# Performance work log

Measured on AMD Instinct MI355X. Metric: run time of the kernel, lower is better.

## Reference

```python
import jax, jax.numpy as jnp
import numpy as np

N, E, ET = 20000, 200000, 40000
D_IN, H, NEA, HL, OUT = 8, 128, 7, 128, 4
HC = H * NEA  # 896


def _init(k, shape, fan_in):
    return jax.random.normal(k, shape, jnp.float32) * (1.0 / np.sqrt(fan_in))


def setup_inputs() -> dict:
    key = jax.random.key(0)
    ks = list(jax.random.split(key, 16))
    return {
        "x": jax.random.normal(ks[0], (N, D_IN), jnp.float32),
        "edge_index": jax.random.randint(ks[1], (2, E), 0, N),
        "edge_attr": jax.random.uniform(ks[2], (E, NEA), jnp.float32),
        "edge_index_test": jax.random.randint(ks[3], (2, ET), 0, N),
        "W0": _init(ks[4], (NEA, D_IN, H), D_IN), "b0": jnp.zeros((NEA, H), jnp.float32),
        "W1": _init(ks[5], (HC, H), HC), "b1": jnp.zeros((H,), jnp.float32),
        "W2": _init(ks[6], (NEA, H, H), H), "b2": jnp.zeros((NEA, H), jnp.float32),
        "W3": _init(ks[7], (NEA, HC, H), HC), "b3": jnp.zeros((NEA, H), jnp.float32),
        "ew1": _init(ks[8], (NEA, NEA * 4), NEA), "eb1": jnp.zeros((NEA * 4,), jnp.float32),
        "ew2": _init(ks[9], (NEA * 4, NEA * 4), NEA * 4), "eb2": jnp.zeros((NEA * 4,), jnp.float32),
        "ew3": _init(ks[10], (NEA * 4, 1), NEA * 4), "eb3": jnp.zeros((1,), jnp.float32),
        "lw0": _init(ks[11], (2 * HC, HL), 2 * HC), "lb0": jnp.zeros((HL,), jnp.float32),
        "lwh": _init(ks[12], (3, HL, HL), HL), "lbh": jnp.zeros((3, HL), jnp.float32),
        "lw4": _init(ks[13], (HL, OUT), HL), "lb4": jnp.zeros((OUT,), jnp.float32),
    }


def _forward(x, edge_attr, W0, b0, W1, b1, W2, b2, W3, b3,
             ew1, eb1, ew2, eb2, ew3, eb3,
             lw0, lb0, lwh, lbh, lw4, lb4,
             edge_index, edge_index_test):
    n = x.shape[0]
    row, col = edge_index[0], edge_index[1]
    loop = jnp.arange(n)
    # PyG gcn_norm: append self-loops with weight 1
    rows = jnp.concatenate([row, loop])
    cols = jnp.concatenate([col, loop])

    def gcn_norm(w):
        w2 = jnp.concatenate([w, jnp.ones((n,), w.dtype)])
        deg = jax.ops.segment_sum(w2, cols, num_segments=n)
        dis = jnp.where(deg > 0, 1.0 / jnp.sqrt(deg), 0.0)
        return dis[rows] * w2 * dis[cols]  # [E+N]

    norms = [gcn_norm(edge_attr[:, i]) for i in range(NEA)]

    def conv(h, W, b, norm):
        m = (h @ W)[rows] * norm[:, None]  # [E+N, H] gathered messages
        return jax.ops.segment_sum(m, cols, num_segments=n) + b

    x1 = jax.nn.relu(jnp.concatenate([conv(x, W0[i], b0[i], norms[i]) for i in range(NEA)], -1))
    # multi_edge_to_one (edge_fc_layers[1]) -> scalar edge weight in (0,1)
    t = jax.nn.relu(edge_attr @ ew1 + eb1)
    t = jax.nn.relu(t @ ew2 + eb2)
    ew = jax.nn.sigmoid((t @ ew3 + eb3)[:, 0])
    x2 = jax.nn.relu(conv(x1, W1, b1, gcn_norm(ew)))
    x3 = jax.nn.relu(jnp.concatenate([conv(x2, W2[i], b2[i], norms[i]) for i in range(NEA)], -1))
    x4 = jax.nn.relu(jnp.concatenate([conv(x3, W3[i], b3[i], norms[i]) for i in range(NEA)], -1))
    # dropout(p=0.5) is identity in eval mode

    def link_mlp(e):
        h = jax.nn.relu(e @ lw0 + lb0)
        for i in range(3):
            h = jax.nn.relu(h @ lwh[i] + lbh[i])
        return h @ lw4 + lb4

    s, d = edge_index_test[0], edge_index_test[1]
    t1 = link_mlp(jnp.concatenate([x4[s], x4[d]], -1))
    t2 = link_mlp(jnp.concatenate([x4[d], x4[s]], -1))[:, jnp.array([0, 2, 1, 3])]
    return 0.5 * (t1 + t2)  # [E_test, 4]


def reference(x, edge_index, edge_attr, edge_index_test,
              W0, b0, W1, b1, W2, b2, W3, b3,
              ew1, eb1, ew2, eb2, ew3, eb3,
              lw0, lb0, lwh, lbh, lw4, lb4):
    return _forward(x, edge_attr, W0, b0, W1, b1, W2, b2, W3, b3,
                    ew1, eb1, ew2, eb2, ew3, eb3,
                    lw0, lb0, lwh, lbh, lw4, lb4,
                    edge_index, edge_index_test)
```

## Files before the change

kernel.cpp:

```cpp
#include <hip/hip_runtime.h>
#include <math.h>

#define NN 20000
#define NE 200000
#define NT 40000

typedef _Float16 f16;
typedef __attribute__((ext_vector_type(8))) _Float16 f16x8;
typedef __attribute__((ext_vector_type(4))) float f32x4;
typedef __attribute__((ext_vector_type(2))) _Float16 h2;

__device__ __forceinline__ void split_store_h(float v, f16* hi, f16* lo, size_t idx) {
  f16 h = (f16)v;
  hi[idx] = h;
  lo[idx] = (f16)(v - (float)h);
}

__global__ void k_edge_mlp(const float* __restrict__ ea,
                           const float* __restrict__ w1, const float* __restrict__ b1,
                           const float* __restrict__ w2, const float* __restrict__ b2,
                           const float* __restrict__ w3, const float* __restrict__ b3,
                           float* __restrict__ out) {
  int e = blockIdx.x * 256 + threadIdx.x;
  if (e >= NE) return;
  float a[7];
#pragma unroll
  for (int i = 0; i < 7; i++) a[i] = ea[e * 7 + i];
  float t1[28];
#pragma unroll
  for (int j = 0; j < 28; j++) {
    float s = b1[j];
#pragma unroll
    for (int k = 0; k < 7; k++) s = fmaf(a[k], w1[k * 28 + j], s);
    t1[j] = fmaxf(s, 0.f);
  }
  float t2[28];
  for (int j = 0; j < 28; j++) {
    float s = b2[j];
    for (int k = 0; k < 28; k++) s = fmaf(t1[k], w2[k * 28 + j], s);
    t2[j] = fmaxf(s, 0.f);
  }
  float s = b3[0];
  for (int k = 0; k < 28; k++) s = fmaf(t2[k], w3[k], s);
  out[e] = 1.f / (1.f + expf(-s));
}

__global__ void k_count(const int* __restrict__ col, int* __restrict__ cnt) {
  int e = blockIdx.x * 256 + threadIdx.x;
  if (e < NE) atomicAdd(&cnt[col[e]], 1);
}

__global__ void k_scan(const int* __restrict__ cnt, int* __restrict__ rowptr) {
  __shared__ int sums[256];
  __shared__ int offs[256];
  int t = threadIdx.x;
  const int CH = (NN + 255) / 256;
  int base = t * CH;
  int s = 0;
  for (int i = 0; i < CH; i++) { int idx = base + i; if (idx < NN) s += cnt[idx]; }
  sums[t] = s;
  __syncthreads();
  if (t == 0) {
    int acc = 0;
    for (int i = 0; i < 256; i++) { offs[i] = acc; acc += sums[i]; }
    rowptr[NN] = acc;
  }
  __syncthreads();
  int acc = offs[t];
  for (int i = 0; i < CH; i++) {
    int idx = base + i;
    if (idx < NN) { rowptr[idx] = acc; acc += cnt[idx]; }
  }
}

__global__ void k_copy_i32(const int* __restrict__ src, int* __restrict__ dst, int n) {
  int i = blockIdx.x * 256 + threadIdx.x;
  if (i < n) dst[i] = src[i];
}

__global__ void k_fill_csr(const int* __restrict__ col, int* __restrict__ cursor,
                           int* __restrict__ eid) {
  int e = blockIdx.x * 256 + threadIdx.x;
  if (e >= NE) return;
  int pos = atomicAdd(&cursor[col[e]], 1);
  eid[pos] = e;
}

__global__ __launch_bounds__(64) void k_deg_csr(const int* __restrict__ rowptr,
                                                const int* __restrict__ eid,
                                                const float* __restrict__ ea,
                                                const float* __restrict__ ewb,
                                                float* __restrict__ dis) {
  int t = threadIdx.x;
  int n = blockIdx.x * 8 + (t >> 3);
  int i = t & 7;
  if (n >= NN) return;
  float deg = 1.f;
  int s = rowptr[n], e2 = rowptr[n + 1];
  for (int p = s; p < e2; p++) {
    int e = eid[p];
    deg += (i < 7) ? ea[e * 7 + i] : ewb[e];
  }
  dis[i * NN + n] = rsqrtf(deg);
}

__global__ void k_csr_norms(const int* __restrict__ eid, const int* __restrict__ row,
                            const int* __restrict__ col, const float* __restrict__ ea,
                            const float* __restrict__ ew, const float* __restrict__ dis,
                            int* __restrict__ csr_src, float* __restrict__ csr_norm) {
  int p = blockIdx.x * 256 + threadIdx.x;
  if (p >= NE) return;
  int e = eid[p];
  int r = row[e], c = col[e];
  csr_src[p] = r;
#pragma unroll
  for (int i = 0; i < 7; i++)
    csr_norm[i * NE + p] = dis[i * NN + r] * ea[e * 7 + i] * dis[i * NN + c];
  csr_norm[7 * NE + p] = dis[7 * NN + r] * ew[e] * dis[7 * NN + c];
}

__global__ void k_wprep(const float* __restrict__ W, int ldW, size_t matOff, int K,
                        f16* __restrict__ WT) {
  int g = blockIdx.y;
  int idx = blockIdx.x * 256 + threadIdx.x;
  if (idx >= K * 128) return;
  int k = idx >> 7, n = idx & 127;
  float v = W[(size_t)g * matOff + (size_t)k * ldW + n];
  WT[(size_t)g * 128 * K + (size_t)n * K + k] = (f16)v;
}

template <int OUTM, bool RELU, bool BIAS, bool GROUP_A, bool SWIZZLE>
__global__ __launch_bounds__(256) void k_mgemm(
    const f16* __restrict__ Ahi, const f16* __restrict__ Alo,
    const f16* __restrict__ BT,
    const float* __restrict__ bias,
    float* __restrict__ Cf, f16* __restrict__ Chi, f16* __restrict__ Clo,
    f16* __restrict__ Ch,
    int ldA, int M, int K, int NG, int GXp) {
  int rowT, g;
  if (SWIZZLE) {
    int b = blockIdx.x;
    int xcd = b & 7, s = b >> 3;
    g = s % NG;
    int lr = s / NG;
    rowT = lr * 8 + xcd;
    if (rowT >= GXp) return;
  } else {
    rowT = blockIdx.x;
    g = blockIdx.y;
  }
  __shared__ f16 smem[12288];
  const int tid = threadIdx.x;
  const int w = tid >> 6, lane = tid & 63;
  const int quad = lane >> 4, lc = lane & 15;
  const int wr = w >> 1, wc = w & 1;
  const int bm = rowT * 128;
  const int ldC = NG * 128;
  const int cb = g * 128;
  const int aoff = GROUP_A ? g * K : 0;
  const f16* Bg = BT + (size_t)g * 128 * K;
  const int srow = lane >> 2, skoff = (lane & 3) * 8;

  f32x4 acc[4][4] = {};

  for (int k0 = 0; k0 < K; k0 += 32) {
#pragma unroll
    for (int l = 0; l < 6; l++) {
      int c = w + l * 4;
      int t = c >> 3, r16 = c & 7;
      int rowi = r16 * 16 + srow;
      f16* ldst = smem + t * 4096 + r16 * 512;
      const f16* src;
      if (t < 2) {
        int gm = bm + rowi;
        if (gm > M - 1) gm = M - 1;
        src = (t == 0 ? Ahi : Alo) + (size_t)gm * ldA + aoff + k0 + skoff;
      } else {
        src = Bg + (size_t)rowi * K + k0 + skoff;
      }
      __builtin_amdgcn_global_load_lds(
          (const __attribute__((address_space(1))) void*)src,
          (__attribute__((address_space(3))) void*)ldst, 16, 0, 0);
    }
    __syncthreads();
    f16x8 bf[4];
#pragma unroll
    for (int nt = 0; nt < 4; nt++) {
      int r = wc * 64 + nt * 16 + lc;
      bf[nt] = *(const f16x8*)(smem + 2 * 4096 + r * 32 + quad * 8);
    }
#pragma unroll
    for (int mt = 0; mt < 4; mt++) {
      int r = wr * 64 + mt * 16 + lc;
      f16x8 ah = *(const f16x8*)(smem + 0 * 4096 + r * 32 + quad * 8);
      f16x8 al = *(const f16x8*)(smem + 1 * 4096 + r * 32 + quad * 8);
#pragma unroll
      for (int nt = 0; nt < 4; nt++) {
        acc[mt][nt] = __builtin_amdgcn_mfma_f32_16x16x32_f16(ah, bf[nt], acc[mt][nt], 0, 0, 0);
        acc[mt][nt] = __builtin_amdgcn_mfma_f32_16x16x32_f16(al, bf[nt], acc[mt][nt], 0, 0, 0);
      }
    }
    __syncthreads();
  }

  float bv[4];
  if (BIAS) {
#pragma unroll
    for (int nt = 0; nt < 4; nt++) bv[nt] = bias[cb + wc * 64 + nt * 16 + lc];
  }
#pragma unroll
  for (int mt = 0; mt < 4; mt++) {
#pragma unroll
    for (int r = 0; r < 4; r++) {
      int gm = bm + wr * 64 + mt * 16 + quad * 4 + r;
      if (gm >= M) continue;
#pragma unroll
      for (int nt = 0; nt < 4; nt++) {
        float v = acc[mt][nt][r];
        if (BIAS) v += bv[nt];
        if (RELU) v = fmaxf(v, 0.f);
        size_t idx = (size_t)gm * ldC + cb + wc * 64 + nt * 16 + lc;
        if (OUTM == 1) {
          f16 h = (f16)v;
          Chi[idx] = h;
          Clo[idx] = (f16)(v - (float)h);
        } else if (OUTM == 2) {
          Ch[idx] = (f16)v;
        } else {
          Cf[idx] = v;
        }
      }
    }
  }
}

__global__ __launch_bounds__(448) void k_agg7(const f16* __restrict__ hW,
                                              const float* __restrict__ csr_norm,
                                              const float* __restrict__ dis,
                                              const int* __restrict__ rowptr,
                                              const int* __restrict__ csr_src,
                                              const float* __restrict__ bias,
                                              f16* __restrict__ outhi,
                                              f16* __restrict__ outlo) {
  int n = blockIdx.x;
  int f2 = threadIdx.x;
  int i = f2 >> 6;
  const h2* hw2 = (const h2*)hW;
  const float* nrm = csr_norm + (size_t)i * NE;
  float d = dis[i * NN + n];
  h2 sv = hw2[(size_t)n * 448 + f2];
  float ax = d * d * (float)sv.x, ay = d * d * (float)sv.y;
  int s = rowptr[n], e = rowptr[n + 1];
  int p = s;
  for (; p + 4 <= e; p += 4) {
    int s0 = csr_src[p], s1 = csr_src[p + 1], s2 = csr_src[p + 2], s3 = csr_src[p + 3];
    float n0 = nrm[p], n1 = nrm[p + 1], n2 = nrm[p + 2], n3 = nrm[p + 3];
    h2 v0 = hw2[(size_t)s0 * 448 + f2];
    h2 v1 = hw2[(size_t)s1 * 448 + f2];
    h2 v2 = hw2[(size_t)s2 * 448 + f2];
    h2 v3 = hw2[(size_t)s3 * 448 + f2];
    ax = fmaf(n0, (float)v0.x, ax); ay = fmaf(n0, (float)v0.y, ay);
    ax = fmaf(n1, (float)v1.x, ax); ay = fmaf(n1, (float)v1.y, ay);
    ax = fmaf(n2, (float)v2.x, ax); ay = fmaf(n2, (float)v2.y, ay);
    ax = fmaf(n3, (float)v3.x, ax); ay = fmaf(n3, (float)v3.y, ay);
  }
  for (; p < e; p++) {
    int s0 = csr_src[p];
    float n0 = nrm[p];
    h2 v0 = hw2[(size_t)s0 * 448 + f2];
    ax = fmaf(n0, (float)v0.x, ax); ay = fmaf(n0, (float)v0.y, ay);
  }
  float vx = fmaxf(ax + bias[2 * f2], 0.f);
  float vy = fmaxf(ay + bias[2 * f2 + 1], 0.f);
  split_store_h(vx, outhi, outlo, (size_t)n * 896 + 2 * f2);
  split_store_h(vy, outhi, outlo, (size_t)n * 896 + 2 * f2 + 1);
}

__global__ __launch_bounds__(256) void k_agg1(const f16* __restrict__ hW,
                                              const float* __restrict__ nrm,
                                              const float* __restrict__ dis_i,
                                              const int* __restrict__ rowptr,
                                              const int* __restrict__ csr_src,
                                              const float* __restrict__ bias,
                                              float* __restrict__ x2f) {
  int t = threadIdx.x;
  int n = blockIdx.x * 4 + (t >> 6);
  int f2 = t & 63;
  if (n >= NN) return;
  const h2* hw2 = (const h2*)hW;
  float d = dis_i[n];
  h2 sv = hw2[(size_t)n * 64 + f2];
  float ax = d * d * (float)sv.x, ay = d * d * (float)sv.y;
  int s = rowptr[n], e = rowptr[n + 1];
  int p = s;
  for (; p + 4 <= e; p += 4) {
    int s0 = csr_src[p], s1 = csr_src[p + 1], s2 = csr_src[p + 2], s3 = csr_src[p + 3];
    float n0 = nrm[p], n1 = nrm[p + 1], n2 = nrm[p + 2], n3 = nrm[p + 3];
    h2 v0 = hw2[(size_t)s0 * 64 + f2];
    h2 v1 = hw2[(size_t)s1 * 64 + f2];
    h2 v2 = hw2[(size_t)s2 * 64 + f2];
    h2 v3 = hw2[(size_t)s3 * 64 + f2];
    ax = fmaf(n0, (float)v0.x, ax); ay = fmaf(n0, (float)v0.y, ay);
    ax = fmaf(n1, (float)v1.x, ax); ay = fmaf(n1, (float)v1.y, ay);
    ax = fmaf(n2, (float)v2.x, ax); ay = fmaf(n2, (float)v2.y, ay);
    ax = fmaf(n3, (float)v3.x, ax); ay = fmaf(n3, (float)v3.y, ay);
  }
  for (; p < e; p++) {
    int s0 = csr_src[p];
    float n0 = nrm[p];
    h2 v0 = hw2[(size_t)s0 * 64 + f2];
    ax = fmaf(n0, (float)v0.x, ax); ay = fmaf(n0, (float)v0.y, ay);
  }
  x2f[(size_t)n * 128 + 2 * f2] = fmaxf(ax + bias[2 * f2], 0.f);
  x2f[(size_t)n * 128 + 2 * f2 + 1] = fmaxf(ay + bias[2 * f2 + 1], 0.f);
}

__global__ __launch_bounds__(256) void k_agg2(const float* __restrict__ x2f,
                                              const float* __restrict__ csr_norm,
                                              const float* __restrict__ dis,
                                              const int* __restrict__ rowptr,
                                              const int* __restrict__ csr_src,
                                              f16* __restrict__ ohi,
                                              f16* __restrict__ olo) {
  int t = threadIdx.x;
  int n = blockIdx.x * 4 + (t >> 6);
  int f2 = t & 63;
  if (n >= NN) return;
  const float2* x2 = (const float2*)x2f;
  float2 sv = x2[(size_t)n * 64 + f2];
  float ax[7], ay[7];
#pragma unroll
  for (int i = 0; i < 7; i++) {
    float d = dis[i * NN + n];
    ax[i] = d * d * sv.x;
    ay[i] = d * d * sv.y;
  }
  int s = rowptr[n], e = rowptr[n + 1];
  int p = s;
  for (; p + 2 <= e; p += 2) {
    int s0 = csr_src[p], s1 = csr_src[p + 1];
    float2 v0 = x2[(size_t)s0 * 64 + f2];
    float2 v1 = x2[(size_t)s1 * 64 + f2];
#pragma unroll
    for (int i = 0; i < 7; i++) {
      float n0 = csr_norm[(size_t)i * NE + p];
      float n1 = csr_norm[(size_t)i * NE + p + 1];
      ax[i] = fmaf(n0, v0.x, ax[i]); ay[i] = fmaf(n0, v0.y, ay[i]);
      ax[i] = fmaf(n1, v1.x, ax[i]); ay[i] = fmaf(n1, v1.y, ay[i]);
    }
  }
  for (; p < e; p++) {
    int s0 = csr_src[p];
    float2 v0 = x2[(size_t)s0 * 64 + f2];
#pragma unroll
    for (int i = 0; i < 7; i++) {
      float n0 = csr_norm[(size_t)i * NE + p];
      ax[i] = fmaf(n0, v0.x, ax[i]); ay[i] = fmaf(n0, v0.y, ay[i]);
    }
  }
#pragma unroll
  for (int i = 0; i < 7; i++) {
    split_store_h(ax[i], ohi, olo, (size_t)n * 896 + i * 128 + 2 * f2);
    split_store_h(ay[i], ohi, olo, (size_t)n * 896 + i * 128 + 2 * f2 + 1);
  }
}

__global__ __launch_bounds__(64) void k_agg_x(const float* __restrict__ x,
                                              const float* __restrict__ csr_norm,
                                              const float* __restrict__ dis,
                                              const int* __restrict__ rowptr,
                                              const int* __restrict__ csr_src,
                                              float* __restrict__ xagg) {
  int n = blockIdx.x;
  int f = threadIdx.x;
  if (f >= 56) return;
  int i = f >> 3, c = f & 7;
  float d = dis[i * NN + n];
  float acc = d * d * x[(size_t)n * 8 + c];
  int s = rowptr[n], e = rowptr[n + 1];
  for (int p = s; p < e; p++)
    acc = fmaf(csr_norm[i * NE + p], x[(size_t)csr_src[p] * 8 + c], acc);
  xagg[(size_t)n * 56 + f] = acc;
}

__global__ __launch_bounds__(896) void k_gemm0(const float* __restrict__ xagg,
                                               const float* __restrict__ W0,
                                               const float* __restrict__ b0,
                                               f16* __restrict__ outhi,
                                               f16* __restrict__ outlo) {
  int n = blockIdx.x;
  int f = threadIdx.x;
  int i = f >> 7, h = f & 127;
  float s = b0[i * 128 + h];
#pragma unroll
  for (int c = 0; c < 8; c++)
    s = fmaf(xagg[(size_t)n * 56 + i * 8 + c], W0[(i * 8 + c) * 128 + h], s);
  float v = fmaxf(s, 0.f);
  split_store_h(v, outhi, outlo, (size_t)n * 896 + f);
}

__global__ __launch_bounds__(128) void k_link_gather(const float* __restrict__ UV,
                                                     const int* __restrict__ eit,
                                                     const float* __restrict__ lb0,
                                                     f16* __restrict__ Hhi,
                                                     f16* __restrict__ Hlo) {
  int t = blockIdx.x;
  int f = threadIdx.x;
  int s = eit[t], d = eit[NT + t];
  float b = lb0[f];
  float v1 = fmaxf(UV[(size_t)s * 256 + f] + UV[(size_t)d * 256 + 128 + f] + b, 0.f);
  float v2 = fmaxf(UV[(size_t)d * 256 + f] + UV[(size_t)s * 256 + 128 + f] + b, 0.f);
  split_store_h(v1, Hhi, Hlo, (size_t)t * 128 + f);
  split_store_h(v2, Hhi, Hlo, (size_t)(NT + t) * 128 + f);
}

__global__ void k_link_out(const f16* __restrict__ Hhi, const f16* __restrict__ Hlo,
                           const float* __restrict__ lw4, const float* __restrict__ lb4,
                           float* __restrict__ out) {
  int t = blockIdx.x * 256 + threadIdx.x;
  if (t >= NT) return;
  float o1[4] = {lb4[0], lb4[1], lb4[2], lb4[3]};
  float o2[4] = {o1[0], o1[1], o1[2], o1[3]};
  for (int k = 0; k < 128; k++) {
    size_t i1 = (size_t)t * 128 + k, i2 = (size_t)(NT + t) * 128 + k;
    float h1 = (float)Hhi[i1] + (float)Hlo[i1];
    float h2v = (float)Hhi[i2] + (float)Hlo[i2];
#pragma unroll
    for (int j = 0; j < 4; j++) {
      float w = lw4[k * 4 + j];
      o1[j] = fmaf(h1, w, o1[j]);
      o2[j] = fmaf(h2v, w, o2[j]);
    }
  }
  out[t * 4 + 0] = 0.5f * (o1[0] + o2[0]);
  out[t * 4 + 1] = 0.5f * (o1[1] + o2[2]);
  out[t * 4 + 2] = 0.5f * (o1[2] + o2[1]);
  out[t * 4 + 3] = 0.5f * (o1[3] + o2[3]);
}

extern "C" void kernel_launch(void* const* d_in, const int* in_sizes, int n_in,
                              void* d_out, int out_size, void* d_ws, size_t ws_size,
                              hipStream_t stream) {
  const float* x   = (const float*)d_in[0];
  const int*   ei  = (const int*)d_in[1];
  const float* ea  = (const float*)d_in[2];
  const int*   eit = (const int*)d_in[3];
  const float* W0  = (const float*)d_in[4];
  const float* b0  = (const float*)d_in[5];
  const float* W1  = (const float*)d_in[6];
  const float* b1  = (const float*)d_in[7];
  const float* W2  = (const float*)d_in[8];
  const float* b2  = (const float*)d_in[9];
  const float* W3  = (const float*)d_in[10];
  const float* b3  = (const float*)d_in[11];
  const float* ew1 = (const float*)d_in[12];
  const float* eb1 = (const float*)d_in[13];
  const float* ew2 = (const float*)d_in[14];
  const float* eb2 = (const float*)d_in[15];
  const float* ew3 = (const float*)d_in[16];
  const float* eb3 = (const float*)d_in[17];
  const float* lw0 = (const float*)d_in[18];
  const float* lb0 = (const float*)d_in[19];
  const float* lwh = (const float*)d_in[20];
  const float* lbh = (const float*)d_in[21];
  const float* lw4 = (const float*)d_in[22];
  const float* lb4 = (const float*)d_in[23];
  const int* row = ei;
  const int* col = ei + NE;
  float* out = (float*)d_out;

  char* ws = (char*)d_ws;
  size_t off = 0;
  auto alloc = [&](size_t bytes) -> char* {
    char* p = ws + off;
    off += (bytes + 255) & ~(size_t)255;
    return p;
  };
  f16*   xAhi   = (f16*)alloc((size_t)NN * 896 * 2);
  f16*   xAlo   = (f16*)alloc((size_t)NN * 896 * 2);
  float* xB     = (float*)alloc((size_t)NN * 896 * 4);
  float* x2f    = (float*)alloc((size_t)NN * 128 * 4);
  float* UV     = (float*)alloc((size_t)NN * 256 * 4);
  float* csr_nrm= (float*)alloc((size_t)8 * NE * 4);
  float* dis    = (float*)alloc((size_t)8 * NN * 4);
  float* ewb    = (float*)alloc((size_t)NE * 4);
  int*   rowptr = (int*)alloc((size_t)(NN + 1) * 4);
  int*   cursor = (int*)alloc((size_t)NN * 4);
  int*   eid    = (int*)alloc((size_t)NE * 4);
  int*   csr_src= (int*)alloc((size_t)NE * 4);
  f16* w1t  = (f16*)alloc((size_t)128 * 896 * 2);
  f16* w2t  = (f16*)alloc((size_t)7 * 128 * 128 * 2);
  f16* w3t  = (f16*)alloc((size_t)7 * 128 * 896 * 2);
  f16* lw0t = (f16*)alloc((size_t)2 * 128 * 896 * 2);
  f16* lwht = (f16*)alloc((size_t)3 * 128 * 128 * 2);
  float* xagg = UV;
  (void)ws_size; (void)in_sizes; (void)n_in; (void)out_size;

  const int EB = (NE + 255) / 256;
  const int NB = (NN + 255) / 256;
  const int GX = (NN + 127) / 128;
  const int MC = (GX + 7) / 8;

  k_wprep<<<dim3(448, 1), 256, 0, stream>>>(W1, 128, 0, 896, w1t);
  k_wprep<<<dim3(64, 7), 256, 0, stream>>>(W2, 128, (size_t)128 * 128, 128, w2t);
  k_wprep<<<dim3(448, 7), 256, 0, stream>>>(W3, 128, (size_t)896 * 128, 896, w3t);
  k_wprep<<<dim3(448, 2), 256, 0, stream>>>(lw0, 128, (size_t)896 * 128, 896, lw0t);
  k_wprep<<<dim3(64, 3), 256, 0, stream>>>(lwh, 128, (size_t)128 * 128, 128, lwht);

  k_edge_mlp<<<EB, 256, 0, stream>>>(ea, ew1, eb1, ew2, eb2, ew3, eb3, ewb);
  hipMemsetAsync(cursor, 0, (size_t)NN * 4, stream);
  k_count<<<EB, 256, 0, stream>>>(col, cursor);
  k_scan<<<1, 256, 0, stream>>>(cursor, rowptr);
  k_copy_i32<<<NB, 256, 0, stream>>>(rowptr, cursor, NN);
  k_fill_csr<<<EB, 256, 0, stream>>>(col, cursor, eid);
  k_deg_csr<<<(NN + 7) / 8, 64, 0, stream>>>(rowptr, eid, ea, ewb, dis);
  k_csr_norms<<<EB, 256, 0, stream>>>(eid, row, col, ea, ewb, dis, csr_src, csr_nrm);

  k_agg_x<<<NN, 64, 0, stream>>>(x, csr_nrm, dis, rowptr, csr_src, xagg);
  k_gemm0<<<NN, 896, 0, stream>>>(xagg, W0, b0, xAhi, xAlo);

  f16* hW1 = (f16*)xB;
  k_mgemm<2, false, false, false, false><<<dim3(GX, 1), 256, 0, stream>>>(
      xAhi, xAlo, w1t, nullptr, nullptr, nullptr, nullptr, hW1,
      896, NN, 896, 1, GX);
  k_agg1<<<(NN + 3) / 4, 256, 0, stream>>>(hW1, csr_nrm + (size_t)7 * NE,
                                           dis + (size_t)7 * NN, rowptr, csr_src, b1, x2f);

  f16* xagg2hi = (f16*)xB;
  f16* xagg2lo = xagg2hi + (size_t)NN * 896;
  k_agg2<<<(NN + 3) / 4, 256, 0, stream>>>(x2f, csr_nrm, dis, rowptr, csr_src,
                                           xagg2hi, xagg2lo);
  k_mgemm<1, true, true, true, false><<<dim3(GX, 7), 256, 0, stream>>>(
      xagg2hi, xagg2lo, w2t, b2, nullptr, xAhi, xAlo, nullptr,
      896, NN, 128, 7, GX);

  f16* hW3 = (f16*)xB;
  k_mgemm<2, false, false, false, true><<<dim3(8 * MC * 7), 256, 0, stream>>>(
      xAhi, xAlo, w3t, nullptr, nullptr, nullptr, nullptr, hW3,
      896, NN, 896, 7, GX);
  k_agg7<<<NN, 448, 0, stream>>>(hW3, csr_nrm, dis, rowptr, csr_src, b3, xAhi, xAlo);

  k_mgemm<0, false, false, false, true><<<dim3(8 * MC * 2), 256, 0, stream>>>(
      xAhi, xAlo, lw0t, nullptr, UV, nullptr, nullptr, nullptr,
      896, NN, 896, 2, GX);

  f16* Hahi = (f16*)xB;
  f16* Halo = Hahi + (size_t)2 * NT * 128;
  f16* Hbhi = Halo + (size_t)2 * NT * 128;
  f16* Hblo = Hbhi + (size_t)2 * NT * 128;
  k_link_gather<<<NT, 128, 0, stream>>>(UV, eit, lb0, Hahi, Halo);
  const int LGX = (2 * NT + 127) / 128;
  for (int i = 0; i < 3; i++) {
    const f16* wt = lwht + (size_t)i * 128 * 128;
    const float* bb = lbh + (size_t)i * 128;
    f16* shi = (i % 2 == 0) ? Hahi : Hbhi;
    f16* slo = (i % 2 == 0) ? Halo : Hblo;
    f16* dhi = (i % 2 == 0) ? Hbhi : Hahi;
    f16* dlo = (i % 2 == 0) ? Hblo : Halo;
    k_mgemm<1, true, true, false, false><<<dim3(LGX, 1), 256, 0, stream>>>(
        shi, slo, wt, bb, nullptr, dhi, dlo, nullptr,
        128, 2 * NT, 128, 1, LGX);
  }
  k_link_out<<<(NT + 255) / 256, 256, 0, stream>>>(Hbhi, Hblo, lw4, lb4, out);
}
```

Measured before the change: 702.8 us.

## Fuse link MLP into one shared-memory kernel and merge CSR count steps

Replaces the link gather, three hidden-layer GEMM launches and the output kernel with one fused kernel. Each block keeps its 64 rows of hidden activations in LDS as a hi/lo f16 pair and runs MFMA layers in place, so intermediate activations no longer round-trip through global memory. It also folds the degree-count atomics into the edge MLP kernel and has the scan write the cursor directly, which drops the separate count and copy launches. The cost is lower occupancy from the large LDS footprint and reloading the weights once per block.

```diff
diff --git a/kernel.cpp b/kernel.cpp
--- a/kernel.cpp
+++ b/kernel.cpp
@@ -4,6 +4,7 @@
 #define NN 20000
 #define NE 200000
 #define NT 40000
+#define HP 136
 
 typedef _Float16 f16;
 typedef __attribute__((ext_vector_type(8))) _Float16 f16x8;
@@ -20,9 +21,11 @@
                            const float* __restrict__ w1, const float* __restrict__ b1,
                            const float* __restrict__ w2, const float* __restrict__ b2,
                            const float* __restrict__ w3, const float* __restrict__ b3,
-                           float* __restrict__ out) {
+                           const int* __restrict__ col,
+                           float* __restrict__ out, int* __restrict__ cnt) {
   int e = blockIdx.x * 256 + threadIdx.x;
   if (e >= NE) return;
+  atomicAdd(&cnt[col[e]], 1);
   float a[7];
 #pragma unroll
   for (int i = 0; i < 7; i++) a[i] = ea[e * 7 + i];
@@ -45,12 +48,7 @@
   out[e] = 1.f / (1.f + expf(-s));
 }
 
-__global__ void k_count(const int* __restrict__ col, int* __restrict__ cnt) {
-  int e = blockIdx.x * 256 + threadIdx.x;
-  if (e < NE) atomicAdd(&cnt[col[e]], 1);
-}
-
-__global__ void k_scan(const int* __restrict__ cnt, int* __restrict__ rowptr) {
+__global__ void k_scan(int* __restrict__ cnt, int* __restrict__ rowptr) {
   __shared__ int sums[256];
   __shared__ int offs[256];
   int t = threadIdx.x;
@@ -69,13 +67,13 @@
   int acc = offs[t];
   for (int i = 0; i < CH; i++) {
     int idx = base + i;
-    if (idx < NN) { rowptr[idx] = acc; acc += cnt[idx]; }
-  }
-}
-
-__global__ void k_copy_i32(const int* __restrict__ src, int* __restrict__ dst, int n) {
-  int i = blockIdx.x * 256 + threadIdx.x;
-  if (i < n) dst[i] = src[i];
+    if (idx < NN) {
+      int cv = cnt[idx];
+      rowptr[idx] = acc;
+      cnt[idx] = acc;
+      acc += cv;
+    }
+  }
 }
 
 __global__ void k_fill_csr(const int* __restrict__ col, int* __restrict__ cursor,
@@ -399,43 +397,89 @@
   split_store_h(v, outhi, outlo, (size_t)n * 896 + f);
 }
 
-__global__ __launch_bounds__(128) void k_link_gather(const float* __restrict__ UV,
-                                                     const int* __restrict__ eit,
-                                                     const float* __restrict__ lb0,
-                                                     f16* __restrict__ Hhi,
-                                                     f16* __restrict__ Hlo) {
-  int t = blockIdx.x;
-  int f = threadIdx.x;
-  int s = eit[t], d = eit[NT + t];
-  float b = lb0[f];
-  float v1 = fmaxf(UV[(size_t)s * 256 + f] + UV[(size_t)d * 256 + 128 + f] + b, 0.f);
-  float v2 = fmaxf(UV[(size_t)d * 256 + f] + UV[(size_t)s * 256 + 128 + f] + b, 0.f);
-  split_store_h(v1, Hhi, Hlo, (size_t)t * 128 + f);
-  split_store_h(v2, Hhi, Hlo, (size_t)(NT + t) * 128 + f);
-}
-
-__global__ void k_link_out(const f16* __restrict__ Hhi, const f16* __restrict__ Hlo,
-                           const float* __restrict__ lw4, const float* __restrict__ lb4,
-                           float* __restrict__ out) {
-  int t = blockIdx.x * 256 + threadIdx.x;
-  if (t >= NT) return;
-  float o1[4] = {lb4[0], lb4[1], lb4[2], lb4[3]};
-  float o2[4] = {o1[0], o1[1], o1[2], o1[3]};
-  for (int k = 0; k < 128; k++) {
-    size_t i1 = (size_t)t * 128 + k, i2 = (size_t)(NT + t) * 128 + k;
-    float h1 = (float)Hhi[i1] + (float)Hlo[i1];
-    float h2v = (float)Hhi[i2] + (float)Hlo[i2];
-#pragma unroll
-    for (int j = 0; j < 4; j++) {
-      float w = lw4[k * 4 + j];
-      o1[j] = fmaf(h1, w, o1[j]);
-      o2[j] = fmaf(h2v, w, o2[j]);
-    }
-  }
-  out[t * 4 + 0] = 0.5f * (o1[0] + o2[0]);
-  out[t * 4 + 1] = 0.5f * (o1[1] + o2[2]);
-  out[t * 4 + 2] = 0.5f * (o1[2] + o2[1]);
-  out[t * 4 + 3] = 0.5f * (o1[3] + o2[3]);
+__global__ __launch_bounds__(256) void k_link_fused(
+    const float* __restrict__ UV, const int* __restrict__ eit,
+    const float* __restrict__ lb0, const f16* __restrict__ lwht,
+    const float* __restrict__ lbh, const float* __restrict__ lw4,
+    const float* __restrict__ lb4, float* __restrict__ out) {
+  __shared__ f16 Hhi[64 * HP];
+  __shared__ f16 Hlo[64 * HP];
+  __shared__ f16 Wt[128 * HP];
+  __shared__ float ob[64][4];
+  const int tid = threadIdx.x;
+  const int t0 = blockIdx.x * 32;
+  {
+    int c = tid & 127;
+    int rbase = tid >> 7;
+    for (int it = 0; it < 32; it++) {
+      int rr = rbase + it * 2;
+      int tp = t0 + (rr >> 1), dir = rr & 1;
+      int s = eit[tp], d = eit[NT + tp];
+      int a = dir ? d : s, b = dir ? s : d;
+      float v = UV[(size_t)a * 256 + c] + UV[(size_t)b * 256 + 128 + c] + lb0[c];
+      v = fmaxf(v, 0.f);
+      f16 h = (f16)v;
+      Hhi[rr * HP + c] = h;
+      Hlo[rr * HP + c] = (f16)(v - (float)h);
+    }
+  }
+  const int w = tid >> 6, lane = tid & 63;
+  const int quad = lane >> 4, lc = lane & 15;
+  for (int l = 0; l < 3; l++) {
+    __syncthreads();
+    {
+      const f16* src = lwht + (size_t)l * 128 * 128;
+#pragma unroll
+      for (int it = 0; it < 8; it++) {
+        int idx = (tid + it * 256) * 8;
+        int n = idx >> 7, k = idx & 127;
+        *(float4*)&Wt[n * HP + k] = *(const float4*)&src[idx];
+      }
+    }
+    __syncthreads();
+    f32x4 acc[8] = {};
+    const int arow = w * 16 + lc;
+#pragma unroll
+    for (int k0 = 0; k0 < 128; k0 += 32) {
+      f16x8 ah = *(const f16x8*)&Hhi[arow * HP + k0 + quad * 8];
+      f16x8 al = *(const f16x8*)&Hlo[arow * HP + k0 + quad * 8];
+#pragma unroll
+      for (int nt = 0; nt < 8; nt++) {
+        f16x8 bf = *(const f16x8*)&Wt[(nt * 16 + lc) * HP + k0 + quad * 8];
+        acc[nt] = __builtin_amdgcn_mfma_f32_16x16x32_f16(ah, bf, acc[nt], 0, 0, 0);
+        acc[nt] = __builtin_amdgcn_mfma_f32_16x16x32_f16(al, bf, acc[nt], 0, 0, 0);
+      }
+    }
+#pragma unroll
+    for (int nt = 0; nt < 8; nt++) {
+      int col = nt * 16 + lc;
+      float bb = lbh[l * 128 + col];
+#pragma unroll
+      for (int r = 0; r < 4; r++) {
+        int rrow = w * 16 + quad * 4 + r;
+        float v = fmaxf(acc[nt][r] + bb, 0.f);
+        f16 h = (f16)v;
+        Hhi[rrow * HP + col] = h;
+        Hlo[rrow * HP + col] = (f16)(v - (float)h);
+      }
+    }
+  }
+  __syncthreads();
+  {
+    int rr = tid >> 2, j = tid & 3;
+    float o = lb4[j];
+    for (int k = 0; k < 128; k++) {
+      float hv = (float)Hhi[rr * HP + k] + (float)Hlo[rr * HP + k];
+      o = fmaf(hv, lw4[k * 4 + j], o);
+    }
+    ob[rr][j] = o;
+  }
+  __syncthreads();
+  if (tid < 128) {
+    int tp = tid >> 2, j = tid & 3;
+    const int perm[4] = {0, 2, 1, 3};
+    out[(size_t)(t0 + tp) * 4 + j] = 0.5f * (ob[2 * tp][j] + ob[2 * tp + 1][perm[j]]);
+  }
 }
 
 extern "C" void kernel_launch(void* const* d_in, const int* in_sizes, int n_in,
@@ -497,7 +541,6 @@
   (void)ws_size; (void)in_sizes; (void)n_in; (void)out_size;
 
   const int EB = (NE + 255) / 256;
-  const int NB = (NN + 255) / 256;
   const int GX = (NN + 127) / 128;
   const int MC = (GX + 7) / 8;
 
@@ -507,11 +550,9 @@
   k_wprep<<<dim3(448, 2), 256, 0, stream>>>(lw0, 128, (size_t)896 * 128, 896, lw0t);
   k_wprep<<<dim3(64, 3), 256, 0, stream>>>(lwh, 128, (size_t)128 * 128, 128, lwht);
 
-  k_edge_mlp<<<EB, 256, 0, stream>>>(ea, ew1, eb1, ew2, eb2, ew3, eb3, ewb);
   hipMemsetAsync(cursor, 0, (size_t)NN * 4, stream);
-  k_count<<<EB, 256, 0, stream>>>(col, cursor);
+  k_edge_mlp<<<EB, 256, 0, stream>>>(ea, ew1, eb1, ew2, eb2, ew3, eb3, col, ewb, cursor);
   k_scan<<<1, 256, 0, stream>>>(cursor, rowptr);
-  k_copy_i32<<<NB, 256, 0, stream>>>(rowptr, cursor, NN);
   k_fill_csr<<<EB, 256, 0, stream>>>(col, cursor, eid);
   k_deg_csr<<<(NN + 7) / 8, 64, 0, stream>>>(rowptr, eid, ea, ewb, dis);
   k_csr_norms<<<EB, 256, 0, stream>>>(eid, row, col, ea, ewb, dis, csr_src, csr_nrm);
@@ -544,22 +585,5 @@
       xAhi, xAlo, lw0t, nullptr, UV, nullptr, nullptr, nullptr,
       896, NN, 896, 2, GX);
 
-  f16* Hahi = (f16*)xB;
-  f16* Halo = Hahi + (size_t)2 * NT * 128;
-  f16* Hbhi = Halo + (size_t)2 * NT * 128;
-  f16* Hblo = Hbhi + (size_t)2 * NT * 128;
-  k_link_gather<<<NT, 128, 0, stream>>>(UV, eit, lb0, Hahi, Halo);
-  const int LGX = (2 * NT + 127) / 128;
-  for (int i = 0; i < 3; i++) {
-    const f16* wt = lwht + (size_t)i * 128 * 128;
-    const float* bb = lbh + (size_t)i * 128;
-    f16* shi = (i % 2 == 0) ? Hahi : Hbhi;
-    f16* slo = (i % 2 == 0) ? Halo : Hblo;
-    f16* dhi = (i % 2 == 0) ? Hbhi : Hahi;
-    f16* dlo = (i % 2 == 0) ? Hblo : Halo;
-    k_mgemm<1, true, true, false, false><<<dim3(LGX, 1), 256, 0, stream>>>(
-        shi, slo, wt, bb, nullptr, dhi, dlo, nullptr,
-        128, 2 * NT, 128, 1, LGX);
-  }
-  k_link_out<<<(NT + 255) / 256, 256, 0, stream>>>(Hbhi, Hblo, lw4, lb4, out);
-}
+  k_link_fused<<<NT / 32, 256, 0, stream>>>(UV, eit, lb0, lwht, lbh, lw4, lb4, out);
+}
```

Result: faster. 658.7 us (-6.3%).
